# Optimization experiments

Hardware: AMD Instinct MI355X
Metric: run time of the kernel (lower is better)

Reference implementation:

```python
import jax, jax.numpy as jnp
import numpy as np

OUT, IN, R = 8192, 8192, 16
GROUP = 16
SCALING = 16.0 / 16.0  # lora_alpha / r
# nvfp4 (e2m1) code table: 3 low bits magnitude, bit 3 = sign
NVFP4_LUT = jnp.array([0.0, 0.5, 1.0, 1.5, 2.0, 3.0, 4.0, 6.0,
                       -0.0, -0.5, -1.0, -1.5, -2.0, -3.0, -4.0, -6.0],
                      dtype=jnp.float32)


def setup_inputs() -> dict:
    key = jax.random.key(0)
    k1, k2, k3, k4, k5 = jax.random.split(key, 5)
    x = jax.random.normal(k1, (64, IN), dtype=jnp.float32)
    packed_weight = jax.random.randint(k2, (OUT, IN // 2), 0, 256, dtype=jnp.int32).astype(jnp.uint8)
    # effective block scales (global scale already absorbed, as in _load_prequantized_nvfp4)
    weight_block_scales = (jax.random.uniform(k3, (OUT, IN // GROUP), dtype=jnp.float32) + 0.1) * 0.01
    lora_A = jax.random.normal(k4, (R, IN), dtype=jnp.float32) * (1.0 / np.sqrt(IN))
    lora_B = jax.random.normal(k5, (OUT, R), dtype=jnp.float32) * 0.01
    return {"x": x, "packed_weight": packed_weight,
            "weight_block_scales": weight_block_scales,
            "lora_A": lora_A, "lora_B": lora_B}


def _dequant_nvfp4(packed, block_scales):
    # packed: (OUT, IN//2) uint8, two fp4 codes per byte (low nibble = even index)
    low = (packed & 0xF).astype(jnp.int32)
    high = (packed >> 4).astype(jnp.int32)
    codes = jnp.stack([low, high], axis=-1).reshape(packed.shape[0], -1)  # (OUT, IN)
    vals = NVFP4_LUT[codes]
    O, I = vals.shape
    # per-block scale over groups of GROUP along in_features
    W = (vals.reshape(O, I // GROUP, GROUP) * block_scales[:, :, None]).reshape(O, I)
    return W


def reference(x, packed_weight, weight_block_scales, lora_A, lora_B):
    W = _dequant_nvfp4(packed_weight, weight_block_scales)      # (OUT, IN) fp32
    base = x @ W.T                                              # (B, OUT)
    lora = (x @ lora_A.T) @ lora_B.T                            # (B, OUT)
    return base + SCALING * lora
```

## Files before the change

kernel.cpp:

```cpp
#include <hip/hip_runtime.h>
#include <stdint.h>

#define IN_F   8192
#define OUT_F  8192
#define MB     64
#define RANK   16
#define KSPLIT 16

typedef _Float16 f16x8 __attribute__((ext_vector_type(8)));
typedef _Float16 f16x2 __attribute__((ext_vector_type(2)));
typedef float    f32x4 __attribute__((ext_vector_type(4)));

__device__ __forceinline__ unsigned pk2h(float a, float b) {
    return __builtin_bit_cast(unsigned, __builtin_amdgcn_cvt_pkrtz(a, b));
}

__device__ __forceinline__ f16x8 decode8(unsigned p, unsigned s2) {
    unsigned q  = p >> 4;
    unsigned me = __builtin_amdgcn_perm(0x46444240u, 0x3E3C3800u, p & 0x07070707u);
    unsigned mo = __builtin_amdgcn_perm(0x46444240u, 0x3E3C3800u, q & 0x07070707u);
    unsigned he = ((p & 0x08080808u) << 4) | me;
    unsigned ho = ((q & 0x08080808u) << 4) | mo;
    unsigned bu0 = __builtin_amdgcn_perm(ho, he, 0x040C000Cu);
    unsigned bu1 = __builtin_amdgcn_perm(ho, he, 0x050C010Cu);
    unsigned bu2 = __builtin_amdgcn_perm(ho, he, 0x060C020Cu);
    unsigned bu3 = __builtin_amdgcn_perm(ho, he, 0x070C030Cu);
    f16x2 sv = __builtin_bit_cast(f16x2, s2);
    f16x2 h0 = __builtin_bit_cast(f16x2, bu0) * sv;
    f16x2 h1 = __builtin_bit_cast(f16x2, bu1) * sv;
    f16x2 h2 = __builtin_bit_cast(f16x2, bu2) * sv;
    f16x2 h3 = __builtin_bit_cast(f16x2, bu3) * sv;
    f16x8 b;
    b[0]=h0[0]; b[1]=h0[1]; b[2]=h1[0]; b[3]=h1[1];
    b[4]=h2[0]; b[5]=h2[1]; b[6]=h3[0]; b[7]=h3[1];
    return b;
}

__device__ __forceinline__ unsigned pack4(uint4 a) {
    unsigned t0 = __builtin_amdgcn_perm(a.y, a.x, 0x0C0C0400u);
    unsigned t1 = __builtin_amdgcn_perm(a.w, a.z, 0x0C0C0400u);
    return __builtin_amdgcn_perm(t1, t0, 0x05040100u);
}

__global__ __launch_bounds__(256) void prep_kernel(
    const float* __restrict__ x, const float* __restrict__ lora_A,
    uint2* __restrict__ xf2, float* __restrict__ tp)
{
    const int m = blockIdx.x, kq = blockIdx.y;
    const int tid = threadIdx.x;
    const int mt = m >> 4, l15 = m & 15;
    float acc[RANK];
#pragma unroll
    for (int r = 0; r < RANK; ++r) acc[r] = 0.f;

    const float4* x4 = (const float4*)(x + (size_t)m * IN_F);
    const float4* A4 = (const float4*)lora_A;
#pragma unroll
    for (int it = 0; it < 2; ++it) {
        int j = kq * 512 + it * 256 + tid;
        float4 xv = x4[j];
        uint2 u;
        u.x = pk2h(xv.x, xv.y);
        u.y = pk2h(xv.z, xv.w);
        int kstep = j >> 3, quad = (j >> 1) & 3, h = j & 1;
        xf2[(size_t)(((kstep * 4 + mt) * 64 + quad * 16 + l15) * 2 + h)] = u;
#pragma unroll
        for (int r = 0; r < RANK; ++r) {
            float4 av = A4[(size_t)r * (IN_F / 4) + j];
            acc[r] += xv.x * av.x + xv.y * av.y + xv.z * av.z + xv.w * av.w;
        }
    }
#pragma unroll
    for (int r = 0; r < RANK; ++r)
#pragma unroll
        for (int off = 32; off > 0; off >>= 1)
            acc[r] += __shfl_down(acc[r], off);

    __shared__ float red[4][RANK];
    int lane = tid & 63, wid = tid >> 6;
    if (lane == 0) {
#pragma unroll
        for (int r = 0; r < RANK; ++r) red[wid][r] = acc[r];
    }
    __syncthreads();
    if (tid < RANK)
        tp[((size_t)kq * MB + m) * RANK + tid] =
            red[0][tid] + red[1][tid] + red[2][tid] + red[3][tid];
}

__device__ __forceinline__ float4 lora4(const float* __restrict__ tp, int m,
                                        const float* __restrict__ lora_B, int n4) {
    float ta[RANK];
#pragma unroll
    for (int r = 0; r < RANK; ++r) ta[r] = 0.f;
#pragma unroll
    for (int kq = 0; kq < 4; ++kq) {
        const float4* t4 = (const float4*)(tp + ((size_t)kq * MB + m) * RANK);
#pragma unroll
        for (int i = 0; i < 4; ++i) {
            float4 v = t4[i];
            ta[4*i+0] += v.x; ta[4*i+1] += v.y; ta[4*i+2] += v.z; ta[4*i+3] += v.w;
        }
    }
    float4 o;
    float* op = (float*)&o;
#pragma unroll
    for (int j = 0; j < 4; ++j) {
        const float4* B4 = (const float4*)(lora_B + (size_t)(n4 + j) * RANK);
        float s = 0.f;
#pragma unroll
        for (int i = 0; i < 4; ++i) {
            float4 b = B4[i];
            s += ta[4*i+0]*b.x + ta[4*i+1]*b.y + ta[4*i+2]*b.z + ta[4*i+3]*b.w;
        }
        op[j] = s;
    }
    return o;
}

__global__ __launch_bounds__(256) void lora_kernel(
    const float* __restrict__ tp, const float* __restrict__ lora_B,
    float* __restrict__ out)
{
    const int gid = blockIdx.x * 256 + threadIdx.x;
    ((float4*)out)[gid] = lora4(tp, gid >> 11, lora_B, (gid & 2047) * 4);
}

__global__ __launch_bounds__(256) void finish_kernel(
    const float* __restrict__ partial, const float* __restrict__ tp,
    const float* __restrict__ lora_B, float* __restrict__ out)
{
    const int gid = blockIdx.x * 256 + threadIdx.x;
    float4 p = {0.f, 0.f, 0.f, 0.f};
#pragma unroll
    for (int ksp = 0; ksp < KSPLIT; ++ksp) {
        float4 v = ((const float4*)partial)[(size_t)ksp * (MB * OUT_F / 4) + gid];
        p.x += v.x; p.y += v.y; p.z += v.z; p.w += v.w;
    }
    float4 l = lora4(tp, gid >> 11, lora_B, (gid & 2047) * 4);
    p.x += l.x; p.y += l.y; p.z += l.z; p.w += l.w;
    ((float4*)out)[gid] = p;
}

template<int ATOMIC>
__global__ __launch_bounds__(512, 2) void main7_kernel(
    const void*  __restrict__ Wpv,
    const float* __restrict__ scales,
    const uint4* __restrict__ xf4,
    float*       __restrict__ dst)
{
    __shared__ __align__(16) uint4    xs[4096];
    __shared__ __align__(16) unsigned wlds[8][32][64];

    const int tid = threadIdx.x;
    const int lane = tid & 63, w = tid >> 6;
    const int l15 = lane & 15, quad = lane >> 4, qh = quad >> 1;
    const int ks = blockIdx.x, by = blockIdx.y;
    const int n0 = by * 256 + w * 32;
    const int lr8 = lane >> 3, lc8 = lane & 7;
    const int lr2 = lane >> 1, lc2 = lane & 1;

    unsigned dv = ((const unsigned*)Wpv)[lane];
    const bool fmt1 = (__ballot(dv > 255u) == 0ull);

    const uint4* Wp4 = (const uint4*)Wpv;
    uint4 lt[16];

#define LOADW(h)                                                              \
    do {                                                                      \
        if (fmt1) {                                                           \
            _Pragma("unroll") for (int p = 0; p < 4; ++p)                     \
            _Pragma("unroll") for (int i = 0; i < 4; ++i)                     \
                lt[p * 4 + i] = Wp4[(size_t)(n0 + p * 8 + lr8) * 1024         \
                                    + ks * 64 + (h) * 32 + i * 8 + lc8];      \
        } else {                                                              \
            _Pragma("unroll") for (int i = 0; i < 4; ++i)                     \
                lt[i] = Wp4[(size_t)(n0 + lr2) * 256                          \
                            + ks * 16 + (h) * 8 + i * 2 + lc2];              \
        }                                                                     \
    } while (0)

#define WRITEW(h)                                                             \
    do {                                                                      \
        if (fmt1) {                                                           \
            _Pragma("unroll") for (int p = 0; p < 4; ++p) {                   \
                int rl = p * 8 + lr8, sw = (rl & 7) << 2;                     \
                _Pragma("unroll") for (int i = 0; i < 4; ++i)                 \
                    wlds[w][rl][((h) * 32 + i * 8 + lc8) ^ sw]                \
                        = pack4(lt[p * 4 + i]);                               \
            }                                                                 \
        } else {                                                              \
            int rl = lr2, sw = (rl & 7) << 2;                                 \
            _Pragma("unroll") for (int i = 0; i < 4; ++i) {                   \
                int d0 = ((h) * 8 + i * 2 + lc2) * 4;                         \
                wlds[w][rl][(d0 + 0) ^ sw] = lt[i].x;                         \
                wlds[w][rl][(d0 + 1) ^ sw] = lt[i].y;                         \
                wlds[w][rl][(d0 + 2) ^ sw] = lt[i].z;                         \
                wlds[w][rl][(d0 + 3) ^ sw] = lt[i].w;                         \
            }                                                                 \
        }                                                                     \
    } while (0)

    uint4 xr[8];
    {
        const uint4* gsrc = xf4 + (size_t)ks * 4096;
#pragma unroll
        for (int i = 0; i < 8; ++i) xr[i] = gsrc[i * 512 + tid];
    }
    LOADW(0);

    unsigned sreg[2][16];
#pragma unroll
    for (int nt = 0; nt < 2; ++nt) {
        const float4* sp = (const float4*)(scales
                           + (size_t)(n0 + nt * 16 + l15) * (IN_F / 16) + ks * 32);
#pragma unroll
        for (int i = 0; i < 8; ++i) {
            float4 vv = sp[i];
            float a = qh ? vv.y : vv.x, b = qh ? vv.w : vv.z;
            sreg[nt][2 * i]     = pk2h(a, a);
            sreg[nt][2 * i + 1] = pk2h(b, b);
        }
    }

#pragma unroll
    for (int i = 0; i < 8; ++i) xs[i * 512 + tid] = xr[i];
    WRITEW(0);
    __syncthreads();

    f32x4 acc[4][2];
#pragma unroll
    for (int mt = 0; mt < 4; ++mt)
#pragma unroll
        for (int nt = 0; nt < 2; ++nt)
            acc[mt][nt] = (f32x4){0.f, 0.f, 0.f, 0.f};

    LOADW(1);

#define COMPUTE(h)                                                            \
    do {                                                                      \
        _Pragma("unroll") for (int sc = 0; sc < 8; ++sc) {                    \
            const int s = (h) * 8 + sc;                                       \
            f16x8 afr[4];                                                     \
            _Pragma("unroll") for (int mt = 0; mt < 4; ++mt)                  \
                afr[mt] = __builtin_bit_cast(f16x8, xs[(s * 4 + mt) * 64 + lane]); \
            _Pragma("unroll") for (int nt = 0; nt < 2; ++nt) {                \
                int rl = nt * 16 + l15;                                       \
                unsigned p = wlds[w][rl][(s * 4 + quad) ^ ((rl & 7) << 2)];   \
                f16x8 b = decode8(p, sreg[nt][s]);                            \
                _Pragma("unroll") for (int mt = 0; mt < 4; ++mt)              \
                    acc[mt][nt] = __builtin_amdgcn_mfma_f32_16x16x32_f16(     \
                        afr[mt], b, acc[mt][nt], 0, 0, 0);                    \
            }                                                                 \
        }                                                                     \
    } while (0)

    COMPUTE(0);
    WRITEW(1);
    COMPUTE(1);

#undef LOADW
#undef WRITEW
#undef COMPUTE

    if (ATOMIC == 0) {
        float* pb = dst + (size_t)ks * (MB * OUT_F);
#pragma unroll
        for (int mt = 0; mt < 4; ++mt)
#pragma unroll
            for (int nt = 0; nt < 2; ++nt)
#pragma unroll
                for (int r = 0; r < 4; ++r)
                    pb[(size_t)(mt * 16 + quad * 4 + r) * OUT_F
                       + n0 + nt * 16 + l15] = acc[mt][nt][r];
    } else {
#pragma unroll
        for (int mt = 0; mt < 4; ++mt)
#pragma unroll
            for (int nt = 0; nt < 2; ++nt)
#pragma unroll
                for (int r = 0; r < 4; ++r)
                    atomicAdd(&dst[(size_t)(mt * 16 + quad * 4 + r) * OUT_F
                                   + n0 + nt * 16 + l15], acc[mt][nt][r]);
    }
}

extern "C" void kernel_launch(void* const* d_in, const int* in_sizes, int n_in,
                              void* d_out, int out_size, void* d_ws, size_t ws_size,
                              hipStream_t stream)
{
    (void)in_sizes; (void)n_in; (void)out_size;
    const float* x      = (const float*)d_in[0];
    const void*  Wp     = (const void*)d_in[1];
    const float* scales = (const float*)d_in[2];
    const float* lora_A = (const float*)d_in[3];
    const float* lora_B = (const float*)d_in[4];
    float* out = (float*)d_out;

    char* ws = (char*)d_ws;
    float* tp      = (float*)ws;
    uint2* xf      = (uint2*)(ws + 65536);
    float* partial = (float*)(ws + (2u << 20));
    const bool full = ws_size >= ((size_t)34 << 20);

    prep_kernel<<<dim3(64, 4), 256, 0, stream>>>(x, lora_A, xf, tp);

    if (full) {
        main7_kernel<0><<<dim3(KSPLIT, 32), 512, 0, stream>>>(
            Wp, scales, (const uint4*)xf, partial);
        finish_kernel<<<(MB * OUT_F / 4) / 256, 256, 0, stream>>>(
            partial, tp, lora_B, out);
    } else {
        lora_kernel<<<(MB * OUT_F / 4) / 256, 256, 0, stream>>>(tp, lora_B, out);
        main7_kernel<1><<<dim3(KSPLIT, 32), 512, 0, stream>>>(
            Wp, scales, (const uint4*)xf, out);
    }
}
```

Measured before the change: 233.9 us.

## Fuse x fp16 conversion and LoRA-A projection into main GEMM kernel

Removes the separate prep kernel on the full-workspace path. Each main block now reads fp32 x directly, converts it to fp16 and swizzles it into LDS. The by==0 blocks also compute the per-k-split x·A^T partials, which finish_kernel sums over all KSPLIT slices. This saves one launch and the intermediate xf buffer round trip. In exchange, every block re-converts its x slice, and the LoRA partial work makes the by==0 blocks longer, which may create tail imbalance.

```diff
diff --git a/kernel.cpp b/kernel.cpp
--- a/kernel.cpp
+++ b/kernel.cpp
@@ -44,11 +44,10 @@
 
 __global__ __launch_bounds__(256) void prep_kernel(
     const float* __restrict__ x, const float* __restrict__ lora_A,
-    uint2* __restrict__ xf2, float* __restrict__ tp)
+    float* __restrict__ tp)
 {
     const int m = blockIdx.x, kq = blockIdx.y;
     const int tid = threadIdx.x;
-    const int mt = m >> 4, l15 = m & 15;
     float acc[RANK];
 #pragma unroll
     for (int r = 0; r < RANK; ++r) acc[r] = 0.f;
@@ -59,11 +58,6 @@
     for (int it = 0; it < 2; ++it) {
         int j = kq * 512 + it * 256 + tid;
         float4 xv = x4[j];
-        uint2 u;
-        u.x = pk2h(xv.x, xv.y);
-        u.y = pk2h(xv.z, xv.w);
-        int kstep = j >> 3, quad = (j >> 1) & 3, h = j & 1;
-        xf2[(size_t)(((kstep * 4 + mt) * 64 + quad * 16 + l15) * 2 + h)] = u;
 #pragma unroll
         for (int r = 0; r < RANK; ++r) {
             float4 av = A4[(size_t)r * (IN_F / 4) + j];
@@ -88,13 +82,14 @@
             red[0][tid] + red[1][tid] + red[2][tid] + red[3][tid];
 }
 
+template<int NP>
 __device__ __forceinline__ float4 lora4(const float* __restrict__ tp, int m,
                                         const float* __restrict__ lora_B, int n4) {
     float ta[RANK];
 #pragma unroll
     for (int r = 0; r < RANK; ++r) ta[r] = 0.f;
 #pragma unroll
-    for (int kq = 0; kq < 4; ++kq) {
+    for (int kq = 0; kq < NP; ++kq) {
         const float4* t4 = (const float4*)(tp + ((size_t)kq * MB + m) * RANK);
 #pragma unroll
         for (int i = 0; i < 4; ++i) {
@@ -123,7 +118,7 @@
     float* __restrict__ out)
 {
     const int gid = blockIdx.x * 256 + threadIdx.x;
-    ((float4*)out)[gid] = lora4(tp, gid >> 11, lora_B, (gid & 2047) * 4);
+    ((float4*)out)[gid] = lora4<4>(tp, gid >> 11, lora_B, (gid & 2047) * 4);
 }
 
 __global__ __launch_bounds__(256) void finish_kernel(
@@ -137,17 +132,19 @@
         float4 v = ((const float4*)partial)[(size_t)ksp * (MB * OUT_F / 4) + gid];
         p.x += v.x; p.y += v.y; p.z += v.z; p.w += v.w;
     }
-    float4 l = lora4(tp, gid >> 11, lora_B, (gid & 2047) * 4);
+    float4 l = lora4<KSPLIT>(tp, gid >> 11, lora_B, (gid & 2047) * 4);
     p.x += l.x; p.y += l.y; p.z += l.z; p.w += l.w;
     ((float4*)out)[gid] = p;
 }
 
 template<int ATOMIC>
-__global__ __launch_bounds__(512, 2) void main7_kernel(
+__global__ __launch_bounds__(512, 2) void main9_kernel(
     const void*  __restrict__ Wpv,
     const float* __restrict__ scales,
-    const uint4* __restrict__ xf4,
-    float*       __restrict__ dst)
+    const float* __restrict__ x,
+    const float* __restrict__ lora_A,
+    float*       __restrict__ dst,
+    float*       __restrict__ tp)
 {
     __shared__ __align__(16) uint4    xs[4096];
     __shared__ __align__(16) unsigned wlds[8][32][64];
@@ -201,13 +198,23 @@
         }                                                                     \
     } while (0)
 
-    uint4 xr[8];
+    LOADW(0);
+
     {
-        const uint4* gsrc = xf4 + (size_t)ks * 4096;
-#pragma unroll
-        for (int i = 0; i < 8; ++i) xr[i] = gsrc[i * 512 + tid];
-    }
-    LOADW(0);
+        const float4* xb = (const float4*)x;
+        uint2* xs2 = (uint2*)xs;
+#pragma unroll 4
+        for (int i = 0; i < 16; ++i) {
+            int idx = i * 512 + tid;
+            int m = idx >> 7, c = idx & 127;
+            float4 xv = xb[(size_t)m * (IN_F / 4) + ks * 128 + c];
+            int ksl = c >> 3, qd = (c >> 1) & 3, h = c & 1;
+            uint2 u;
+            u.x = pk2h(xv.x, xv.y);
+            u.y = pk2h(xv.z, xv.w);
+            xs2[(size_t)(((ksl * 4 + (m >> 4)) * 64 + qd * 16 + (m & 15)) * 2 + h)] = u;
+        }
+    }
 
     unsigned sreg[2][16];
 #pragma unroll
@@ -223,8 +230,6 @@
         }
     }
 
-#pragma unroll
-    for (int i = 0; i < 8; ++i) xs[i * 512 + tid] = xr[i];
     WRITEW(0);
     __syncthreads();
 
@@ -283,6 +288,24 @@
                     atomicAdd(&dst[(size_t)(mt * 16 + quad * 4 + r) * OUT_F
                                    + n0 + nt * 16 + l15], acc[mt][nt][r]);
     }
+
+    if (ATOMIC == 0 && by == 0 && tid < 256) {
+        const int m = tid >> 2, rq = (tid & 3) * 4;
+        const float4* xr4 = (const float4*)x + (size_t)m * (IN_F / 4) + ks * 128;
+        const float4* A4  = (const float4*)lora_A;
+        float ar[4] = {0.f, 0.f, 0.f, 0.f};
+#pragma unroll 8
+        for (int c = 0; c < 128; ++c) {
+            float4 xv = xr4[c];
+#pragma unroll
+            for (int rr = 0; rr < 4; ++rr) {
+                float4 av = A4[(size_t)(rq + rr) * (IN_F / 4) + ks * 128 + c];
+                ar[rr] += xv.x * av.x + xv.y * av.y + xv.z * av.z + xv.w * av.w;
+            }
+        }
+        float4 o = {ar[0], ar[1], ar[2], ar[3]};
+        *(float4*)&tp[((size_t)ks * MB + m) * RANK + rq] = o;
+    }
 }
 
 extern "C" void kernel_launch(void* const* d_in, const int* in_sizes, int n_in,
@@ -299,20 +322,18 @@
 
     char* ws = (char*)d_ws;
     float* tp      = (float*)ws;
-    uint2* xf      = (uint2*)(ws + 65536);
-    float* partial = (float*)(ws + (2u << 20));
+    float* partial = (float*)(ws + (1u << 20));
     const bool full = ws_size >= ((size_t)34 << 20);
 
-    prep_kernel<<<dim3(64, 4), 256, 0, stream>>>(x, lora_A, xf, tp);
-
     if (full) {
-        main7_kernel<0><<<dim3(KSPLIT, 32), 512, 0, stream>>>(
-            Wp, scales, (const uint4*)xf, partial);
+        main9_kernel<0><<<dim3(KSPLIT, 32), 512, 0, stream>>>(
+            Wp, scales, x, lora_A, partial, tp);
         finish_kernel<<<(MB * OUT_F / 4) / 256, 256, 0, stream>>>(
             partial, tp, lora_B, out);
     } else {
+        prep_kernel<<<dim3(64, 4), 256, 0, stream>>>(x, lora_A, tp);
         lora_kernel<<<(MB * OUT_F / 4) / 256, 256, 0, stream>>>(tp, lora_B, out);
-        main7_kernel<1><<<dim3(KSPLIT, 32), 512, 0, stream>>>(
-            Wp, scales, (const uint4*)xf, out);
-    }
-}
+        main9_kernel<1><<<dim3(KSPLIT, 32), 512, 0, stream>>>(
+            Wp, scales, x, lora_A, out, tp);
+    }
+}
```

New measurement: 263.5 us. +12.7%, slower.
